# Performance work log

Measured on AMD Instinct MI355X. Metric: run time of the kernel, lower is better.

## Reference

```python
import jax, jax.numpy as jnp
import numpy as np

D_MODEL = 2048
NUM_GROUPS = 16
D_HEAD = D_MODEL // NUM_GROUPS
ROTARY_DIM = int(D_MODEL * 0.25)  # 512


def setup_inputs() -> dict:
    key = jax.random.key(0)
    ks = jax.random.split(key, 8)
    B, S, N = 4, 2048, 2048
    scale = 1.0 / np.sqrt(D_MODEL)
    return {
        "query": jax.random.normal(ks[0], (B, S, D_MODEL), jnp.float32),
        "key": jax.random.normal(ks[1], (B, N, D_MODEL), jnp.float32),
        "value": jax.random.normal(ks[2], (B, N, D_MODEL), jnp.float32),
        "mask": jax.random.randint(ks[3], (B, S), 0, 2, jnp.int32),
        "position_ids": jnp.arange(S, dtype=jnp.int64) if jax.config.jax_enable_x64 else jnp.arange(S, dtype=jnp.int32),
        "Wq": jax.random.normal(ks[4], (D_MODEL, D_MODEL), jnp.float32) * scale,
        "Wk": jax.random.normal(ks[5], (D_MODEL, D_MODEL), jnp.float32) * scale,
        "Wv": jax.random.normal(ks[6], (D_MODEL, D_MODEL), jnp.float32) * scale,
        "Wo": jax.random.normal(ks[7], (D_MODEL, D_MODEL), jnp.float32) * scale,
    }


def _apply_rope_query_only(q, k, position_ids):
    # Faithful to source: rotary embedding is applied to query ONLY; key is returned unchanged.
    rd = ROTARY_DIM
    pos = position_ids.astype(q.dtype)  # (S,)
    freq = jnp.arange(0, rd, 2, dtype=q.dtype)
    inv_freq = 1.0 / (10000.0 ** (freq / rd))  # (rd/2,)
    pe = pos[:, None] * inv_freq[None, :]       # (S, rd/2)
    cos = jnp.tile(jnp.cos(pe), (1, 2))[None]   # (1, S, rd) tiled [c, c]
    sin = jnp.tile(jnp.sin(pe), (1, 2))[None]
    q_rot, q_pass = q[..., :rd], q[..., rd:]
    half = rd // 2
    q_rot_half = jnp.concatenate([-q_rot[..., half:], q_rot[..., :half]], axis=-1)
    q_rot = q_rot * cos + q_rot_half * sin
    q = jnp.concatenate([q_rot, q_pass], axis=-1)
    return q, k


def reference(query, key, value, mask, position_ids, Wq, Wk, Wv, Wo):
    B, S, _ = query.shape
    N = key.shape[1]
    G, dh = NUM_GROUPS, D_HEAD

    q = query @ Wq.T
    k = key @ Wk.T
    v = value @ Wv.T

    q, k = _apply_rope_query_only(q, k, position_ids)

    qh = q.reshape(B, S, G, dh).transpose(0, 2, 1, 3)  # (B,G,S,dh)
    kh = k.reshape(B, N, G, dh).transpose(0, 2, 1, 3)  # (B,G,N,dh)
    vh = v.reshape(B, N, G, dh).transpose(0, 2, 1, 3)  # (B,G,N,dh)

    scores = jnp.einsum("bgsd,bgnd->bgsn", qh, kh) / jnp.sqrt(jnp.asarray(dh, q.dtype))
    # mask (B,S) -> (B,1,1,N); here S == N so pad width is 0 (pad value 1 in source)
    m = mask[:, None, None, :]
    scores = jnp.where(m == 0, -jnp.inf, scores)

    w = jax.nn.softmax(scores, axis=-1)
    out = jnp.einsum("bgsn,bgnd->bgsd", w, vh)           # (B,G,S,dh)
    out = out.transpose(0, 2, 1, 3).reshape(B, S, D_MODEL)
    return out @ Wo.T
```

## Files before the change

kernel.cpp:

```cpp
#include <hip/hip_runtime.h>
#include <hip/hip_bf16.h>
#include <type_traits>
#include <utility>

typedef unsigned short u16;
typedef unsigned int u32;
typedef __attribute__((ext_vector_type(8))) short  s16x8;
typedef __attribute__((ext_vector_type(4))) short  s16x4;
typedef __attribute__((ext_vector_type(4))) float  f32x4;
typedef __attribute__((ext_vector_type(16))) float f32x16;
typedef __bf16 bf16x8_t __attribute__((ext_vector_type(8)));
typedef __bf16 bf16x2_t __attribute__((ext_vector_type(2)));

#define SEQ 2048
#define DMODEL 2048
#define NBATCH 4
#define DH 128
#define NB (NBATCH * SEQ)

#define QK_SCALE_LOG2 0.12754375f
#define BIAS_VALID  (-34.624681f)
#define BIAS_MASKED (-180.0f)

#if __has_builtin(__builtin_amdgcn_exp2f)
#define EXP2(x) __builtin_amdgcn_exp2f(x)
#else
#define EXP2(x) exp2f(x)
#endif

#define BARRIER __builtin_amdgcn_s_barrier()
#define FENCE asm volatile("" ::: "memory")
#define VMCNT8 asm volatile("s_waitcnt vmcnt(8)" ::: "memory")
#define VMCNT0 asm volatile("s_waitcnt vmcnt(0)" ::: "memory")

static __device__ __forceinline__ u16 f2bf(float f) {
  unsigned u = __float_as_uint(f);
  u += 0x7fffu + ((u >> 16) & 1u);
  return (u16)(u >> 16);
}
static __device__ __forceinline__ float bf2f(u16 h) {
  return __uint_as_float(((unsigned)h) << 16);
}
static __device__ __forceinline__ u32 pack_bf16(float a, float b) {
  bf16x2_t t; t[0] = (__bf16)a; t[1] = (__bf16)b;
  return __builtin_bit_cast(u32, t);
}
static __device__ __forceinline__ void plswap(u32& a, u32& b) {
  asm("v_permlane32_swap_b32 %0, %1" : "+v"(a), "+v"(b));
}

template <typename T, typename = void>
struct mfma_takes : std::false_type {};
template <typename T>
struct mfma_takes<T, std::void_t<decltype(__builtin_amdgcn_mfma_f32_16x16x32_bf16(
    std::declval<T>(), std::declval<T>(), std::declval<f32x4>(), 0, 0, 0))>>
    : std::true_type {};
using mfma_frag_t = std::conditional_t<mfma_takes<s16x8>::value, s16x8, bf16x8_t>;

static __device__ __forceinline__ f32x16 mfma32(s16x8 a, s16x8 b, f32x16 c) {
  return __builtin_amdgcn_mfma_f32_32x32x16_bf16(
      __builtin_bit_cast(mfma_frag_t, a), __builtin_bit_cast(mfma_frag_t, b), c, 0, 0, 0);
}

typedef const void __attribute__((address_space(1)))* gas_ptr;
typedef void __attribute__((address_space(3)))* las_ptr;
static __device__ __forceinline__ void gload16(const void* g, void* l) {
  __builtin_amdgcn_global_load_lds((gas_ptr)g, (las_ptr)l, 16, 0, 0);
}

static __device__ __forceinline__ s16x8 frag_from_words(u32 w0, u32 w1, u32 w2, u32 w3) {
  union { u32 w[4]; s16x8 v; } u;
  u.w[0] = w0; u.w[1] = w1; u.w[2] = w2; u.w[3] = w3;
  return u.v;
}

static __device__ __forceinline__ void cvt8(const float* src, u16* dst, int i) {
  const float4* p = (const float4*)src + (size_t)i * 2;
  float4 a = p[0], b4 = p[1];
  s16x8 o;
  o[0] = (short)f2bf(a.x);  o[1] = (short)f2bf(a.y);
  o[2] = (short)f2bf(a.z);  o[3] = (short)f2bf(a.w);
  o[4] = (short)f2bf(b4.x); o[5] = (short)f2bf(b4.y);
  o[6] = (short)f2bf(b4.z); o[7] = (short)f2bf(b4.w);
  *(s16x8*)(dst + (size_t)i * 8) = o;
}

__global__ void cvt3_k(const float* __restrict__ a, const float* __restrict__ b,
                       const float* __restrict__ c, u16* __restrict__ oa,
                       u16* __restrict__ ob, u16* __restrict__ oc) {
  const int n8 = 1 << 21;
  const int stride = (int)(gridDim.x * blockDim.x);
  for (int i = (int)(blockIdx.x * blockDim.x + threadIdx.x); i < 3 * n8; i += stride) {
    const int seg = i >> 21, off = i & (n8 - 1);
    const float* src = seg == 0 ? a : (seg == 1 ? b : c);
    u16* dst = seg == 0 ? oa : (seg == 1 ? ob : oc);
    cvt8(src, dst, off);
  }
}

__global__ void cvt4_k(const float* __restrict__ a, const float* __restrict__ b,
                       const float* __restrict__ c, const float* __restrict__ d,
                       u16* __restrict__ oa, u16* __restrict__ ob,
                       u16* __restrict__ oc, u16* __restrict__ od) {
  const int n8 = 1 << 19;
  const int stride = (int)(gridDim.x * blockDim.x);
  for (int i = (int)(blockIdx.x * blockDim.x + threadIdx.x); i < 4 * n8; i += stride) {
    const int seg = i >> 19, off = i & (n8 - 1);
    const float* src = seg == 0 ? a : (seg == 1 ? b : (seg == 2 ? c : d));
    u16* dst = seg == 0 ? oa : (seg == 1 ? ob : (seg == 2 ? oc : od));
    cvt8(src, dst, off);
  }
}

__global__ void bias_k(const int* __restrict__ mask, u16* __restrict__ biasv, int n) {
  const int i = (int)(blockIdx.x * blockDim.x + threadIdx.x);
  if (i < n) biasv[i] = mask[i] ? f2bf(BIAS_VALID) : f2bf(BIAS_MASKED);
}

template <int OUT_MODE>
__global__ __launch_bounds__(512, 2) void gemm256_k(const u16* __restrict__ A,
                                                    const u16* __restrict__ Bw,
                                                    void* __restrict__ Cv) {
  constexpr int M = 8192, N = 2048, K = 2048;
  constexpr int NT = K / 64;
  __shared__ u16 Ab[2][256 * 64];
  __shared__ u16 Bb[2][256 * 64];

  const int tid = (int)threadIdx.x;
  const int wv = tid >> 6, lane = tid & 63;
  const int l32 = lane & 31, hi = lane >> 5;
  const int wm = wv >> 2, wn = wv & 3;

  const int bid = (int)blockIdx.x;
  const int bn = bid & 7, bm = bid >> 3;

  const size_t arow0 = (size_t)bm * 256;
  const size_t brow0 = (size_t)bn * 256;

  const int srow = tid >> 3;
  const int scolb = (tid & 7) * 16;
  const int scol = (scolb ^ ((srow & 7) << 4)) >> 1;
  const u16* agp = A  + (arow0 + srow) * (size_t)K + scol;
  const u16* bgp = Bw + (brow0 + srow) * (size_t)K + scol;

  f32x16 acc[4][2];
#pragma unroll
  for (int mi = 0; mi < 4; ++mi)
#pragma unroll
    for (int ni = 0; ni < 2; ++ni)
#pragma unroll
      for (int r = 0; r < 16; ++r) acc[mi][ni][r] = 0.f;

  auto STAGE8 = [&](int kt2, u16* bufA, u16* bufB) {
#pragma unroll
    for (int j = 0; j < 4; ++j)
      gload16(agp + (size_t)(j * 64) * K + kt2, bufA + (j * 64 + wv * 8) * 64);
#pragma unroll
    for (int j = 0; j < 4; ++j)
      gload16(bgp + (size_t)(j * 64) * K + kt2, bufB + (j * 64 + wv * 8) * 64);
  };
  auto LDA = [&](const u16* buf, int qm, s16x8* af) {
#pragma unroll
    for (int mb = 0; mb < 2; ++mb) {
      const int row = wm * 128 + qm * 64 + mb * 32 + l32;
#pragma unroll
      for (int ks = 0; ks < 4; ++ks) {
        const int cb = ((ks * 32 + hi * 16) ^ ((row & 7) << 4)) >> 1;
        af[mb * 4 + ks] = *(const s16x8*)&buf[row * 64 + cb];
      }
    }
  };
  auto LDB = [&](const u16* buf, int qn, s16x8* bfr) {
    const int row = wn * 64 + qn * 32 + l32;
#pragma unroll
    for (int ks = 0; ks < 4; ++ks) {
      const int cb = ((ks * 32 + hi * 16) ^ ((row & 7) << 4)) >> 1;
      bfr[ks] = *(const s16x8*)&buf[row * 64 + cb];
    }
  };
  auto MM = [&](const s16x8* af, const s16x8* bfr, int qm, int qn) {
    __builtin_amdgcn_s_setprio(1);
#pragma unroll
    for (int mb = 0; mb < 2; ++mb)
#pragma unroll
      for (int ks = 0; ks < 4; ++ks)
        acc[qm * 2 + mb][qn] = mfma32(af[mb * 4 + ks], bfr[ks], acc[qm * 2 + mb][qn]);
    __builtin_amdgcn_s_setprio(0);
  };

  STAGE8(0, Ab[0], Bb[0]);

  for (int t = 0; t < NT; ++t) {
    u16* Ac = Ab[t & 1];
    u16* Bc = Bb[t & 1];
    if (t < NT - 1) {
      STAGE8((t + 1) * 64, Ab[(t + 1) & 1], Bb[(t + 1) & 1]);
      VMCNT8;
    } else {
      VMCNT0;
    }
    BARRIER; FENCE;
    s16x8 af0[8], af1[8], bf0[4], bf1[4];
    LDA(Ac, 0, af0); LDB(Bc, 0, bf0); LDB(Bc, 1, bf1);
    FENCE;
    MM(af0, bf0, 0, 0);
    LDA(Ac, 1, af1);
    MM(af0, bf1, 0, 1);
    MM(af1, bf1, 1, 1);
    MM(af1, bf0, 1, 0);
    BARRIER; FENCE;
  }

  const size_t row0 = arow0 + (size_t)wm * 128;
  const size_t col0 = brow0 + (size_t)wn * 64;
#pragma unroll
  for (int mi = 0; mi < 4; ++mi)
#pragma unroll
    for (int ni = 0; ni < 2; ++ni) {
      const size_t rbase = row0 + mi * 32 + 4 * hi;
      const size_t c = col0 + ni * 32 + l32;
      if constexpr (OUT_MODE == 0) {
        u16* C = (u16*)Cv;
#pragma unroll
        for (int q = 0; q < 4; ++q)
#pragma unroll
          for (int rr = 0; rr < 4; ++rr)
            C[(rbase + 8 * q + rr) * N + c] = f2bf(acc[mi][ni][q * 4 + rr]);
      } else if constexpr (OUT_MODE == 1) {
        float* C = (float*)Cv;
#pragma unroll
        for (int q = 0; q < 4; ++q)
#pragma unroll
          for (int rr = 0; rr < 4; ++rr)
            C[(rbase + 8 * q + rr) * N + c] = acc[mi][ni][q * 4 + rr];
      } else {
        u16* C = (u16*)Cv;
#pragma unroll
        for (int q = 0; q < 4; ++q) {
          s16x4 v;
#pragma unroll
          for (int rr = 0; rr < 4; ++rr) v[rr] = (short)f2bf(acc[mi][ni][q * 4 + rr]);
          *(s16x4*)&C[c * (size_t)M + rbase + 8 * q] = v;
        }
      }
    }
}

__global__ void rope_k(u16* __restrict__ qb, const int* __restrict__ pos_ids) {
  const int row = (int)blockIdx.x;
  const int s = row & (SEQ - 1);
  const int t = (int)threadIdx.x;
  const float pos = (float)pos_ids[s];
  const float ang = pos * exp2f((float)t * (-13.287712379549449f / 256.0f));
  float sn, cs;
  sincosf(ang, &sn, &cs);
  u16* p = qb + (size_t)row * DMODEL;
  const float x = bf2f(p[t]);
  const float y = bf2f(p[t + 256]);
  p[t]       = f2bf((x * cs - y * sn) * QK_SCALE_LOG2);
  p[t + 256] = f2bf((y * cs + x * sn) * QK_SCALE_LOG2);
#pragma unroll
  for (int j = 0; j < 6; ++j) {
    const int d = 512 + t + 256 * j;
    p[d] = f2bf(bf2f(p[d]) * QK_SCALE_LOG2);
  }
}

__device__ __forceinline__ void attn_stage(u16* Ks, u16* Vs,
                                           const u16* kbase, const u16* vbase,
                                           int kt, int w, int lane) {
#pragma unroll
  for (int i = 0; i < 4; ++i) {
    const int row = w * 16 + i * 4 + (lane >> 4);
    const int srcb = ((lane & 15) * 16) ^ ((row & 7) << 4);
    gload16(kbase + (size_t)(kt + row) * DMODEL + (srcb >> 1), &Ks[(w * 16 + i * 4) * 128]);
  }
#pragma unroll
  for (int i = 0; i < 4; ++i) {
    const int row = w * 32 + i * 8 + (lane >> 3);
    const int srcb = ((lane & 7) * 16) ^ ((row & 7) << 4);
    gload16(vbase + (size_t)row * NB + kt + (srcb >> 1), &Vs[(w * 32 + i * 8) * 64]);
  }
}

__global__ __launch_bounds__(256) void attn_k(const u16* __restrict__ q,
                                              const u16* __restrict__ k,
                                              const u16* __restrict__ vt,
                                              const u16* __restrict__ biasv,
                                              u16* __restrict__ att) {
  __shared__ u16 Ks[2][64 * 128];
  __shared__ u16 Vs[2][128 * 64];

  const int tid = (int)threadIdx.x;
  const int w = tid >> 6, lane = tid & 63;
  const int l32 = lane & 31, hi = lane >> 5;

  const int bid = (int)blockIdx.x;
  const int sb = (bid & 7) * 128 + (bid >> 3);
  const int qt = sb & 15;
  const int bg = sb >> 4;
  const int b = bg >> 4, g = bg & 15;

  const int qrow = qt * 128 + w * 32 + l32;
  const u16* qp = q + ((size_t)b * SEQ + qrow) * DMODEL + g * DH;
  s16x8 aq[8];
#pragma unroll
  for (int s = 0; s < 8; ++s) aq[s] = *(const s16x8*)(qp + s * 16 + hi * 8);

  const u32 one0 = (hi == 0) ? 0x00003F80u : 0u;
  const s16x8 bones = frag_from_words(one0, 0, 0, 0);
  const s16x8 allones = frag_from_words(0x3F803F80u, 0x3F803F80u, 0x3F803F80u, 0x3F803F80u);

  f32x16 oacc[4], lacc;
#pragma unroll
  for (int r = 0; r < 16; ++r) {
    lacc[r] = 0.f;
#pragma unroll
    for (int d0 = 0; d0 < 4; ++d0) oacc[d0][r] = 0.f;
  }

  const u16* kbase = k + (size_t)b * SEQ * DMODEL + g * DH;
  const u16* vbase = vt + (size_t)(g * DH) * NB + (size_t)b * SEQ;
  const u16* bbase = biasv + b * SEQ;

  attn_stage(Ks[0], Vs[0], kbase, vbase, 0, w, lane);
  u16 bb0 = bbase[l32], bb1 = bbase[32 + l32];

  for (int t = 0; t < 32; ++t) {
    const int cur = t & 1;
    __syncthreads();
    u16 bbn0 = bb0, bbn1 = bb1;
    if (t < 31) {
      attn_stage(Ks[cur ^ 1], Vs[cur ^ 1], kbase, vbase, (t + 1) * 64, w, lane);
      bbn0 = bbase[(t + 1) * 64 + l32];
      bbn1 = bbase[(t + 1) * 64 + 32 + l32];
    }
    const u16* KsC = Ks[cur];
    const u16* VsC = Vs[cur];

    const s16x8 ab0 = frag_from_words((hi == 0) ? (u32)bb0 : 0u, 0, 0, 0);
    const s16x8 ab1 = frag_from_words((hi == 0) ? (u32)bb1 : 0u, 0, 0, 0);
    __builtin_amdgcn_s_setprio(1);
    f32x16 sacc0 = mfma32(ab0, bones, (f32x16)(0.f));
    f32x16 sacc1 = mfma32(ab1, bones, (f32x16)(0.f));

#pragma unroll
    for (int s = 0; s < 8; ++s) {
      const int byteoff = ((s * 32 + hi * 16) ^ ((l32 & 7) << 4)) >> 1;
      const s16x8 a0 = *(const s16x8*)&KsC[l32 * 128 + byteoff];
      const s16x8 a1 = *(const s16x8*)&KsC[(32 + l32) * 128 + byteoff];
      sacc0 = mfma32(a0, aq[s], sacc0);
      sacc1 = mfma32(a1, aq[s], sacc1);
    }
    __builtin_amdgcn_s_setprio(0);

    u32 pk0[8], pk1[8];
#pragma unroll
    for (int i = 0; i < 8; ++i) {
      pk0[i] = pack_bf16(EXP2(sacc0[2 * i]), EXP2(sacc0[2 * i + 1]));
      pk1[i] = pack_bf16(EXP2(sacc1[2 * i]), EXP2(sacc1[2 * i + 1]));
    }
    s16x8 pa[4];
#pragma unroll
    for (int grp = 0; grp < 4; ++grp) {
      u32* pk = (grp < 2) ? pk0 : pk1;
      const int o = (grp & 1) * 4;
      plswap(pk[o + 0], pk[o + 2]);
      plswap(pk[o + 1], pk[o + 3]);
      pa[grp] = frag_from_words(pk[o + 0], pk[o + 1], pk[o + 2], pk[o + 3]);
    }

    __builtin_amdgcn_s_setprio(1);
#pragma unroll
    for (int ks = 0; ks < 4; ++ks) lacc = mfma32(pa[ks], allones, lacc);

#pragma unroll
    for (int d0 = 0; d0 < 4; ++d0) {
      const int rowd = d0 * 32 + l32;
#pragma unroll
      for (int ks = 0; ks < 4; ++ks) {
        const int byteoff = ((ks * 32 + hi * 16) ^ ((rowd & 7) << 4)) >> 1;
        const s16x8 bv = *(const s16x8*)&VsC[rowd * 64 + byteoff];
        oacc[d0] = mfma32(pa[ks], bv, oacc[d0]);
      }
    }
    __builtin_amdgcn_s_setprio(0);
    bb0 = bbn0; bb1 = bbn1;
  }

  float rinv[16];
#pragma unroll
  for (int r = 0; r < 16; ++r) rinv[r] = 1.0f / lacc[r];
  u16* ob = att + ((size_t)b * SEQ + qt * 128 + w * 32) * DMODEL + g * DH;
#pragma unroll
  for (int d0 = 0; d0 < 4; ++d0)
#pragma unroll
    for (int r = 0; r < 16; ++r) {
      const int qloc = (r & 3) + 8 * (r >> 2) + 4 * hi;
      ob[(size_t)qloc * DMODEL + d0 * 32 + l32] = f2bf(oacc[d0][r] * rinv[r]);
    }
}

extern "C" void kernel_launch(void* const* d_in, const int* in_sizes, int n_in,
                              void* d_out, int out_size, void* d_ws, size_t ws_size,
                              hipStream_t stream) {
  const float* query = (const float*)d_in[0];
  const float* key   = (const float*)d_in[1];
  const float* value = (const float*)d_in[2];
  const int*   maskp = (const int*)d_in[3];
  const int*   posp  = (const int*)d_in[4];
  const float* Wq    = (const float*)d_in[5];
  const float* Wk    = (const float*)d_in[6];
  const float* Wv    = (const float*)d_in[7];
  const float* Wo    = (const float*)d_in[8];

  char* ws = (char*)d_ws;
  const size_t MB = 1024ull * 1024ull;
  u16* wq_b = (u16*)(ws + 0 * MB);
  u16* wk_b = (u16*)(ws + 8 * MB);
  u16* wv_b = (u16*)(ws + 16 * MB);
  u16* wo_b = (u16*)(ws + 24 * MB);
  u16* xq   = (u16*)(ws + 32 * MB);
  u16* xk   = (u16*)(ws + 64 * MB);
  u16* xv   = (u16*)(ws + 96 * MB);
  u16* qb   = (u16*)(ws + 128 * MB);
  u16* kb   = (u16*)(ws + 160 * MB);
  u16* vtb  = (u16*)(ws + 192 * MB);
  u16* att  = xq;
  u16* biasv = xk;

  cvt3_k<<<dim3(2048), dim3(256), 0, stream>>>(query, key, value, xq, xk, xv);
  cvt4_k<<<dim3(1024), dim3(256), 0, stream>>>(Wq, Wk, Wv, Wo, wq_b, wk_b, wv_b, wo_b);

  gemm256_k<0><<<dim3(256), dim3(512), 0, stream>>>(xq, wq_b, (void*)qb);
  gemm256_k<0><<<dim3(256), dim3(512), 0, stream>>>(xk, wk_b, (void*)kb);
  gemm256_k<2><<<dim3(256), dim3(512), 0, stream>>>(xv, wv_b, (void*)vtb);

  bias_k<<<dim3((NBATCH * SEQ + 255) / 256), dim3(256), 0, stream>>>(maskp, biasv, NBATCH * SEQ);

  rope_k<<<dim3(NBATCH * SEQ), dim3(256), 0, stream>>>(qb, posp);

  attn_k<<<dim3(1024), dim3(256), 0, stream>>>(qb, kb, vtb, biasv, att);

  gemm256_k<1><<<dim3(256), dim3(512), 0, stream>>>(att, wo_b, d_out);

  (void)in_sizes; (void)n_in; (void)out_size; (void)ws_size;
}
```

Measured before the change: 607.7 us.

## Interleave half-tile global loads with MFMA phases and remap block tile order

Restructures the GEMM main loop so global-to-LDS staging is split into half-tiles issued between the four MFMA phases, with B prefetched two iterations ahead and A one ahead. Each phase is bracketed by barriers and an lgkmcnt wait, in the style of an 8-wave ping-pong schedule. It also remaps block IDs so that consecutive blocks share weight (B) column tiles, which should improve L2 reuse. The added barriers could cost more than the overlap gains, and the B buffer reuse (Bn = Bb[t&1]) relies on the barrier ordering to avoid overwriting data that is still being read.

```diff
diff --git a/kernel.cpp b/kernel.cpp
--- a/kernel.cpp
+++ b/kernel.cpp
@@ -29,8 +29,9 @@
 #endif
 
 #define BARRIER __builtin_amdgcn_s_barrier()
-#define FENCE asm volatile("" ::: "memory")
-#define VMCNT8 asm volatile("s_waitcnt vmcnt(8)" ::: "memory")
+#define FENCE  asm volatile("" ::: "memory")
+#define LGKM0  asm volatile("s_waitcnt lgkmcnt(0)" ::: "memory")
+#define VMCNT4 asm volatile("s_waitcnt vmcnt(4)" ::: "memory")
 #define VMCNT0 asm volatile("s_waitcnt vmcnt(0)" ::: "memory")
 
 static __device__ __forceinline__ u16 f2bf(float f) {
@@ -132,7 +133,8 @@
   const int wm = wv >> 2, wn = wv & 3;
 
   const int bid = (int)blockIdx.x;
-  const int bn = bid & 7, bm = bid >> 3;
+  const int bn = (bid >> 3) & 7;
+  const int bm = (bid & 7) * 4 + (bid >> 6);
 
   const size_t arow0 = (size_t)bm * 256;
   const size_t brow0 = (size_t)bn * 256;
@@ -151,13 +153,19 @@
 #pragma unroll
       for (int r = 0; r < 16; ++r) acc[mi][ni][r] = 0.f;
 
-  auto STAGE8 = [&](int kt2, u16* bufA, u16* bufB) {
-#pragma unroll
-    for (int j = 0; j < 4; ++j)
-      gload16(agp + (size_t)(j * 64) * K + kt2, bufA + (j * 64 + wv * 8) * 64);
-#pragma unroll
-    for (int j = 0; j < 4; ++j)
-      gload16(bgp + (size_t)(j * 64) * K + kt2, bufB + (j * 64 + wv * 8) * 64);
+  auto SH_A = [&](int kt2, u16* bufA, int half) {
+#pragma unroll
+    for (int j = 0; j < 2; ++j) {
+      const int rb = half * 128 + j * 64;
+      gload16(agp + (size_t)rb * K + kt2, bufA + (rb + wv * 8) * 64);
+    }
+  };
+  auto SH_B = [&](int kt2, u16* bufB, int half) {
+#pragma unroll
+    for (int j = 0; j < 2; ++j) {
+      const int rb = half * 128 + j * 64;
+      gload16(bgp + (size_t)rb * K + kt2, bufB + (rb + wv * 8) * 64);
+    }
   };
   auto LDA = [&](const u16* buf, int qm, s16x8* af) {
 #pragma unroll
@@ -188,27 +196,42 @@
     __builtin_amdgcn_s_setprio(0);
   };
 
-  STAGE8(0, Ab[0], Bb[0]);
+  SH_A(0, Ab[0], 0); SH_A(0, Ab[0], 1);
+  SH_B(0, Bb[0], 0); SH_B(0, Bb[0], 1);
+  SH_B(64, Bb[1], 0); SH_B(64, Bb[1], 1);
+  VMCNT4; BARRIER;
 
   for (int t = 0; t < NT; ++t) {
     u16* Ac = Ab[t & 1];
     u16* Bc = Bb[t & 1];
-    if (t < NT - 1) {
-      STAGE8((t + 1) * 64, Ab[(t + 1) & 1], Bb[(t + 1) & 1]);
-      VMCNT8;
-    } else {
-      VMCNT0;
-    }
-    BARRIER; FENCE;
+    u16* An = Ab[(t + 1) & 1];
+    u16* Bn = Bb[t & 1];
+    const int kA = (t + 1) * 64;
+    const int kB = (t + 2) * 64;
+    const bool stA = (t + 1 < NT);
+    const bool stB = (t + 2 < NT);
     s16x8 af0[8], af1[8], bf0[4], bf1[4];
-    LDA(Ac, 0, af0); LDB(Bc, 0, bf0); LDB(Bc, 1, bf1);
-    FENCE;
+
+    LDA(Ac, 0, af0); LDB(Bc, 0, bf0);
+    if (stA) SH_A(kA, An, 0);
+    BARRIER; LGKM0;
     MM(af0, bf0, 0, 0);
+    BARRIER;
+    LDB(Bc, 1, bf1);
+    if (stA) SH_A(kA, An, 1);
+    BARRIER; LGKM0;
+    MM(af0, bf1, 0, 1);
+    BARRIER;
     LDA(Ac, 1, af1);
-    MM(af0, bf1, 0, 1);
+    if (stB) SH_B(kB, Bn, 0);
+    BARRIER; LGKM0;
     MM(af1, bf1, 1, 1);
+    BARRIER;
+    if (stB) { SH_B(kB, Bn, 1); VMCNT4; }
+    else if (stA) { VMCNT0; }
+    BARRIER; LGKM0;
     MM(af1, bf0, 1, 0);
-    BARRIER; FENCE;
+    BARRIER;
   }
 
   const size_t row0 = arow0 + (size_t)wm * 128;
```

Result: no change. 599.2 us (-1.4%).
